# Kernel optimization log

Measured on AMD Instinct MI355X. Metric: run time of the kernel, lower is better.

## Reference

```python
import jax, jax.numpy as jnp
import numpy as np

TOPK = 2
NORM_TOPK = True
SCALE = 1.0
EPS = 1e-9


def setup_inputs() -> dict:
    key = jax.random.key(0)
    ks = jax.random.split(key, 9)
    h, i, E = 2048, 1024, 16
    std = 0.02
    return {
        "x": jax.random.normal(ks[0], (1, 2048, h), jnp.float32),
        "Wr": jax.random.normal(ks[1], (E, h), jnp.float32) * std,
        "bias": jnp.zeros((E,), jnp.float32),
        "Wg": jax.random.normal(ks[2], (E, h, i), jnp.float32) * std,
        "Wu": jax.random.normal(ks[3], (E, h, i), jnp.float32) * std,
        "Wd": jax.random.normal(ks[4], (E, i, h), jnp.float32) * std,
        "sWg": jax.random.normal(ks[5], (h, i), jnp.float32) * std,
        "sWu": jax.random.normal(ks[6], (h, i), jnp.float32) * std,
        "sWd": jax.random.normal(ks[7], (i, h), jnp.float32) * std,
    }


def reference(x, Wr, bias, Wg, Wu, Wd, sWg, sWu, sWd):
    b, s, h = x.shape
    E = Wr.shape[0]
    xt = x.reshape(b * s, h)  # [T, h]

    # Router: softmax over expert logits, then top-k
    logits = xt @ Wr.T + bias  # [T, E]
    probs = jax.nn.softmax(logits, axis=-1)
    topk_val, topk_idx = jax.lax.top_k(probs, TOPK)  # [T, K]
    if NORM_TOPK:
        w = topk_val / (jnp.sum(topk_val, axis=-1, keepdims=True) + EPS)
    else:
        w = topk_val
    w = w * SCALE

    # Dense per-expert SwiGLU (mathematically identical to gather/scatter dispatch)
    g = jnp.einsum('th,ehi->tei', xt, Wg)  # [T, E, i]
    u = jnp.einsum('th,ehi->tei', xt, Wu)
    y = jnp.einsum('tei,eih->teh', jax.nn.silu(g) * u, Wd)  # [T, E, h]

    # Combine: out[t] = sum_k w[t,k] * y[t, idx[t,k]]
    oh = jax.nn.one_hot(topk_idx, E, dtype=x.dtype)  # [T, K, E]
    routed = jnp.einsum('tke,tk,teh->th', oh, w, y)

    # Shared expert (SwiGLU)
    shared = (jax.nn.silu(xt @ sWg) * (xt @ sWu)) @ sWd

    return (routed + shared).reshape(b, s, h)
```

## Files before the change

kernel.cpp:

```cpp
#include <hip/hip_runtime.h>
#include <hip/hip_bf16.h>

#define T_TOK 2048
#define HDIM  2048
#define IDIM  1024
#define NE    16
#define NEX   17
#define NASSIGN (T_TOK*3)
#define TM    64

#define G1_NWG (TM*16)
#define G2_NWG (TM*32)

typedef __attribute__((ext_vector_type(8))) short bf16x8;
typedef __attribute__((ext_vector_type(4))) float f32x4;

#define WAITVM(N) asm volatile("s_waitcnt vmcnt(" #N ")" ::: "memory")
#define WAITLGKM0 asm volatile("s_waitcnt lgkmcnt(0)" ::: "memory")
#define SCHEDB    __builtin_amdgcn_sched_barrier(0)
#define BARRIER   __builtin_amdgcn_s_barrier()

__device__ __forceinline__ unsigned short f2bf(float f) {
    union { float f; unsigned u; } v; v.f = f;
    unsigned r = v.u + 0x7fffu + ((v.u >> 16) & 1u);
    return (unsigned short)(r >> 16);
}
__device__ __forceinline__ unsigned pack2f(float a, float b) {
    __hip_bfloat162 h = __float22bfloat162_rn(float2{a, b});
    unsigned r;
    __builtin_memcpy(&r, &h, 4);
    return r;
}
__device__ __forceinline__ int SW2(int r) { return (r >> 1) & 3; }
__device__ __forceinline__ int lds_off32(int row, int kelem) {
    return (row << 6) + ((((kelem >> 3) ^ SW2(row))) << 4) + ((kelem & 7) << 1);
}
__device__ __forceinline__ f32x4 mfma16(bf16x8 a, bf16x8 b, f32x4 c) {
    return __builtin_amdgcn_mfma_f32_16x16x32_bf16(a, b, c, 0, 0, 0);
}
__device__ __forceinline__ void gload_lds16(const void* g, void* lds) {
    __builtin_amdgcn_global_load_lds(
        (const __attribute__((address_space(1))) unsigned*)g,
        (__attribute__((address_space(3))) unsigned*)lds, 16, 0, 0);
}

__global__ __launch_bounds__(256) void k_cvt(const float* __restrict__ x,
                                             unsigned short* __restrict__ xbf) {
    int i = blockIdx.x * 256 + threadIdx.x;
    float4 v = ((const float4*)x)[i];
    uint2 p{pack2f(v.x, v.y), pack2f(v.z, v.w)};
    ((uint2*)xbf)[i] = p;
}

__global__ void k_router(const float* __restrict__ x, const float* __restrict__ Wr,
                         const float* __restrict__ bias, float* __restrict__ wtok,
                         int* __restrict__ idxtok, int* __restrict__ counts) {
    int t = blockIdx.x;
    int lane = threadIdx.x & 63;
    int wave = threadIdx.x >> 6;
    __shared__ float lg[NE];
    const float4* xr = (const float4*)(x + (size_t)t * HDIM);
    for (int e = wave; e < NE; e += 4) {
        const float4* wr = (const float4*)(Wr + (size_t)e * HDIM);
        float s = 0.f;
        for (int j = lane; j < HDIM / 4; j += 64) {
            float4 a = xr[j], b = wr[j];
            s += a.x*b.x + a.y*b.y + a.z*b.z + a.w*b.w;
        }
        #pragma unroll
        for (int d = 32; d; d >>= 1) s += __shfl_xor(s, d);
        if (lane == 0) lg[e] = s + bias[e];
    }
    __syncthreads();
    if (threadIdx.x == 0) {
        float m = lg[0];
        #pragma unroll
        for (int e = 1; e < NE; e++) m = fmaxf(m, lg[e]);
        float p[NE]; float S = 0.f;
        #pragma unroll
        for (int e = 0; e < NE; e++) { p[e] = expf(lg[e] - m); S += p[e]; }
        int i0 = 0;
        #pragma unroll
        for (int e = 1; e < NE; e++) if (p[e] > p[i0]) i0 = e;
        int i1 = (i0 == 0) ? 1 : 0;
        for (int e = 0; e < NE; e++) if (e != i0 && p[e] > p[i1]) i1 = e;
        float v0 = p[i0] / S, v1 = p[i1] / S;
        float wsum = v0 + v1 + 1e-9f;
        wtok[t*2+0] = v0 / wsum;
        wtok[t*2+1] = v1 / wsum;
        idxtok[t*2+0] = i0;
        idxtok[t*2+1] = i1;
        atomicAdd(&counts[i0], 1);
        atomicAdd(&counts[i1], 1);
    }
}

__global__ void k_scan(const int* __restrict__ counts, int* __restrict__ offs,
                       int* __restrict__ cursor, int4* __restrict__ tiles) {
    if (threadIdx.x == 0) {
        int acc = 0;
        for (int e = 0; e < NEX; e++) {
            offs[e] = acc; cursor[e] = acc;
            acc += (e < NE) ? counts[e] : T_TOK;
        }
        offs[NEX] = acc;
        int nt = 0;
        for (int e = 0; e < NEX; e++) {
            for (int r = offs[e]; r < offs[e+1]; r += 128) {
                tiles[nt] = int4{r, min(128, offs[e+1] - r), e, 0};
                nt++;
            }
        }
        for (; nt < TM; nt++) tiles[nt] = int4{0, 0, 0, 0};
    }
}

__global__ void k_scatter(const int* __restrict__ idxtok, const float* __restrict__ wtok,
                          int* __restrict__ cursor, const int* __restrict__ offs,
                          int* __restrict__ rows, float* __restrict__ wrow) {
    int t = blockIdx.x * blockDim.x + threadIdx.x;
    if (t >= T_TOK) return;
    #pragma unroll
    for (int k = 0; k < 2; k++) {
        int e = idxtok[t*2+k];
        int pos = atomicAdd(&cursor[e], 1);
        rows[pos] = t;
        wrow[pos] = wtok[t*2+k];
    }
    int p16 = offs[NE] + t;
    rows[p16] = t;
    wrow[p16] = 1.0f;
}

__global__ __launch_bounds__(512) void k_gemm1(
        const unsigned short* __restrict__ xbf,
        const float* __restrict__ Wg, const float* __restrict__ Wu,
        const float* __restrict__ sWg, const float* __restrict__ sWu,
        const int4* __restrict__ tiles, const int* __restrict__ rows,
        const float* __restrict__ wrow, unsigned short* __restrict__ act) {
    int bid = blockIdx.x;
    int wg = (bid & 7) * (G1_NWG >> 3) + (bid >> 3);
    int ti = wg & (TM - 1);
    int ct = wg >> 6;

    int4 tl = tiles[ti];
    int nrows = tl.y;
    if (nrows == 0) return;
    int rs = tl.x, e = tl.z;
    const float* wgp = (e < NE) ? Wg + (size_t)e * HDIM * IDIM : sWg;
    const float* wup = (e < NE) ? Wu + (size_t)e * HDIM * IDIM : sWu;
    int n0 = ct * 64;

    __shared__ unsigned short As[2][128 * 32];
    __shared__ unsigned short Bs[2][64 * 32];
    __shared__ unsigned short Us[2][64 * 32];

    int tid = threadIdx.x;
    int l = tid & 63, w = tid >> 6;

    int arow = w * 16 + (l >> 2);
    int rr = rows[rs + min(arow, nrows - 1)];
    const unsigned short* asrc = xbf + (size_t)rr * HDIM + (((l & 3) ^ SW2(arow)) << 3);

    int sm = tid >> 8;
    int sn = tid & 63;
    int skc = (tid >> 6) & 3;
    const float* wsrc = (sm ? wup : wgp) + (size_t)(skc * 8) * IDIM + n0 + sn;
    unsigned short* wdst0 = sm ? Us[0] : Bs[0];
    unsigned short* wdst1 = sm ? Us[1] : Bs[1];
    int swoff = lds_off32(sn, skc * 8);

    int wr = (w >> 2) << 6;
    int wc = (w & 3) << 4;
    int fr = l & 15;
    int fk = (l >> 4) << 3;

    float wA[8], wB[8];
    f32x4 accg[4] = {}, accu[4] = {};
    const int NK = HDIM / 32;

    #define G1_LOADW(DST, KS) do { \
        size_t kb_ = (size_t)(KS) * 32; \
        _Pragma("unroll") \
        for (int j = 0; j < 8; ++j) DST[j] = wsrc[(kb_ + j) * IDIM]; \
    } while (0)
    #define G1_WRITEW(SRC, P) do { \
        uint4 pw_; \
        pw_.x = pack2f(SRC[0], SRC[1]); pw_.y = pack2f(SRC[2], SRC[3]); \
        pw_.z = pack2f(SRC[4], SRC[5]); pw_.w = pack2f(SRC[6], SRC[7]); \
        *(uint4*)((char*)((P) ? wdst1 : wdst0) + swoff) = pw_; \
    } while (0)
    #define G1_MFMA(P) do { \
        bf16x8 a0 = *(const bf16x8*)((const char*)As[P] + lds_off32(wr + fr, fk)); \
        bf16x8 a1 = *(const bf16x8*)((const char*)As[P] + lds_off32(wr + 16 + fr, fk)); \
        bf16x8 a2 = *(const bf16x8*)((const char*)As[P] + lds_off32(wr + 32 + fr, fk)); \
        bf16x8 a3 = *(const bf16x8*)((const char*)As[P] + lds_off32(wr + 48 + fr, fk)); \
        bf16x8 bg = *(const bf16x8*)((const char*)Bs[P] + lds_off32(wc + fr, fk)); \
        bf16x8 bu = *(const bf16x8*)((const char*)Us[P] + lds_off32(wc + fr, fk)); \
        accg[0] = mfma16(a0, bg, accg[0]);  accu[0] = mfma16(a0, bu, accu[0]); \
        accg[1] = mfma16(a1, bg, accg[1]);  accu[1] = mfma16(a1, bu, accu[1]); \
        accg[2] = mfma16(a2, bg, accg[2]);  accu[2] = mfma16(a2, bu, accu[2]); \
        accg[3] = mfma16(a3, bg, accg[3]);  accu[3] = mfma16(a3, bu, accu[3]); \
    } while (0)
    #define G1_STEP(K, CUR, NXT, P) do { \
        gload_lds16(asrc + min((K) + 1, NK - 1) * 32, (char*)As[(P) ^ 1] + w * 1024); \
        SCHEDB; \
        G1_LOADW(NXT, min((K) + 2, NK - 1)); \
        SCHEDB; \
        WAITVM(9);               \
        G1_WRITEW(CUR, (P) ^ 1); \
        G1_MFMA(P); \
        SCHEDB; \
        WAITVM(8);               \
        WAITLGKM0; \
        BARRIER; \
        SCHEDB; \
    } while (0)

    G1_LOADW(wA, 0);
    gload_lds16(asrc, (char*)As[0] + w * 1024);
    SCHEDB;
    G1_LOADW(wB, 1);
    SCHEDB;
    WAITVM(9);
    G1_WRITEW(wA, 0);
    SCHEDB;
    WAITVM(8);
    WAITLGKM0;
    BARRIER;
    SCHEDB;

    for (int k = 0; k < NK; k += 2) {
        G1_STEP(k,     wB, wA, 0);
        G1_STEP(k + 1, wA, wB, 1);
    }
    asm volatile("s_waitcnt vmcnt(0)" ::: "memory");

    int crow = (l >> 4) << 2;
    int ccol = l & 15;
    #pragma unroll
    for (int m = 0; m < 4; ++m) {
        #pragma unroll
        for (int reg = 0; reg < 4; ++reg) {
            int r = wr + m * 16 + crow + reg;
            if (r < nrows) {
                float wv = wrow[rs + r];
                float g = accg[m][reg], u = accu[m][reg];
                act[(size_t)(rs + r) * IDIM + n0 + wc + ccol] =
                    f2bf(g / (1.f + __expf(-g)) * u * wv);
            }
        }
    }
    #undef G1_LOADW
    #undef G1_WRITEW
    #undef G1_MFMA
    #undef G1_STEP
}

__global__ __launch_bounds__(512) void k_gemm2(
        const unsigned short* __restrict__ act,
        const float* __restrict__ Wd, const float* __restrict__ sWd,
        const int4* __restrict__ tiles, const int* __restrict__ rows,
        float* __restrict__ out) {
    int bid = blockIdx.x;
    int wg = (bid & 7) * (G2_NWG >> 3) + (bid >> 3);
    int ti = wg & (TM - 1);
    int ct = wg >> 6;

    int4 tl = tiles[ti];
    int nrows = tl.y;
    if (nrows == 0) return;
    int rs = tl.x, e = tl.z;
    const float* wdp = (e < NE) ? Wd + (size_t)e * IDIM * HDIM : sWd;
    int n0 = ct * 64;

    __shared__ unsigned short As[2][128 * 32];
    __shared__ unsigned short Bs[2][64 * 32];

    int tid = threadIdx.x;
    int l = tid & 63, w = tid >> 6;

    int arow = w * 16 + (l >> 2);
    const unsigned short* asrc =
        act + (size_t)(rs + min(arow, nrows - 1)) * IDIM + (((l & 3) ^ SW2(arow)) << 3);

    int sn = tid & 63;
    int skc = (tid >> 6) & 7;
    const float* wsrc = wdp + (size_t)(skc * 4) * HDIM + n0 + sn;
    int swoff = lds_off32(sn, skc * 4);

    int wr = (w >> 2) << 6;
    int wc = (w & 3) << 4;
    int fr = l & 15;
    int fk = (l >> 4) << 3;

    float wA[4], wB[4];
    f32x4 acc[4] = {};
    const int NK = IDIM / 32;

    #define G2_LOADW(DST, KS) do { \
        size_t kb_ = (size_t)(KS) * 32; \
        _Pragma("unroll") \
        for (int j = 0; j < 4; ++j) DST[j] = wsrc[(kb_ + j) * HDIM]; \
    } while (0)
    #define G2_WRITEW(SRC, P) do { \
        uint2 pw_; \
        pw_.x = pack2f(SRC[0], SRC[1]); pw_.y = pack2f(SRC[2], SRC[3]); \
        *(uint2*)((char*)Bs[P] + swoff) = pw_; \
    } while (0)
    #define G2_MFMA(P) do { \
        bf16x8 a0 = *(const bf16x8*)((const char*)As[P] + lds_off32(wr + fr, fk)); \
        bf16x8 a1 = *(const bf16x8*)((const char*)As[P] + lds_off32(wr + 16 + fr, fk)); \
        bf16x8 a2 = *(const bf16x8*)((const char*)As[P] + lds_off32(wr + 32 + fr, fk)); \
        bf16x8 a3 = *(const bf16x8*)((const char*)As[P] + lds_off32(wr + 48 + fr, fk)); \
        bf16x8 b  = *(const bf16x8*)((const char*)Bs[P] + lds_off32(wc + fr, fk)); \
        acc[0] = mfma16(a0, b, acc[0]); \
        acc[1] = mfma16(a1, b, acc[1]); \
        acc[2] = mfma16(a2, b, acc[2]); \
        acc[3] = mfma16(a3, b, acc[3]); \
    } while (0)
    #define G2_STEP(K, CUR, NXT, P) do { \
        gload_lds16(asrc + min((K) + 1, NK - 1) * 32, (char*)As[(P) ^ 1] + w * 1024); \
        SCHEDB; \
        G2_LOADW(NXT, min((K) + 2, NK - 1)); \
        SCHEDB; \
        WAITVM(5); \
        G2_WRITEW(CUR, (P) ^ 1); \
        G2_MFMA(P); \
        SCHEDB; \
        WAITVM(4); \
        WAITLGKM0; \
        BARRIER; \
        SCHEDB; \
    } while (0)

    G2_LOADW(wA, 0);
    gload_lds16(asrc, (char*)As[0] + w * 1024);
    SCHEDB;
    G2_LOADW(wB, 1);
    SCHEDB;
    WAITVM(5);
    G2_WRITEW(wA, 0);
    SCHEDB;
    WAITVM(4);
    WAITLGKM0;
    BARRIER;
    SCHEDB;

    for (int k = 0; k < NK; k += 2) {
        G2_STEP(k,     wB, wA, 0);
        G2_STEP(k + 1, wA, wB, 1);
    }
    asm volatile("s_waitcnt vmcnt(0)" ::: "memory");

    int crow = (l >> 4) << 2;
    int ccol = l & 15;
    #pragma unroll
    for (int m = 0; m < 4; ++m) {
        #pragma unroll
        for (int reg = 0; reg < 4; ++reg) {
            int r = wr + m * 16 + crow + reg;
            if (r < nrows) {
                atomicAdd(&out[(size_t)rows[rs + r] * HDIM + n0 + wc + ccol], acc[m][reg]);
            }
        }
    }
    #undef G2_LOADW
    #undef G2_WRITEW
    #undef G2_MFMA
    #undef G2_STEP
}

extern "C" void kernel_launch(void* const* d_in, const int* in_sizes, int n_in,
                              void* d_out, int out_size, void* d_ws, size_t ws_size,
                              hipStream_t stream) {
    const float* x    = (const float*)d_in[0];
    const float* Wr   = (const float*)d_in[1];
    const float* bias = (const float*)d_in[2];
    const float* Wg   = (const float*)d_in[3];
    const float* Wu   = (const float*)d_in[4];
    const float* Wd   = (const float*)d_in[5];
    const float* sWg  = (const float*)d_in[6];
    const float* sWu  = (const float*)d_in[7];
    const float* sWd  = (const float*)d_in[8];
    float* out = (float*)d_out;

    char* p = (char*)d_ws;
    int*   counts = (int*)p;                 p += 256;
    int*   offs   = (int*)p;                 p += 256;
    int*   cursor = (int*)p;                 p += 256;
    int4*  tiles  = (int4*)p;                p += TM * sizeof(int4);
    int*   idxtok = (int*)p;                 p += (size_t)T_TOK * 2 * sizeof(int);
    float* wtok   = (float*)p;               p += (size_t)T_TOK * 2 * sizeof(float);
    int*   rows   = (int*)p;                 p += (size_t)NASSIGN * sizeof(int);
    float* wrow   = (float*)p;               p += (size_t)NASSIGN * sizeof(float);
    unsigned short* act = (unsigned short*)p; p += (size_t)NASSIGN * IDIM * sizeof(unsigned short);
    unsigned short* xbf = (unsigned short*)p;

    hipMemsetAsync(counts, 0, 256, stream);
    hipMemsetAsync(d_out, 0, (size_t)out_size * sizeof(float), stream);

    k_cvt<<<dim3(T_TOK * HDIM / 1024), dim3(256), 0, stream>>>(x, xbf);
    k_router<<<dim3(T_TOK), dim3(256), 0, stream>>>(x, Wr, bias, wtok, idxtok, counts);
    k_scan<<<dim3(1), dim3(64), 0, stream>>>(counts, offs, cursor, tiles);
    k_scatter<<<dim3((T_TOK + 255) / 256), dim3(256), 0, stream>>>(idxtok, wtok, cursor, offs, rows, wrow);
    k_gemm1<<<dim3(G1_NWG), dim3(512), 0, stream>>>(xbf, Wg, Wu, sWg, sWu, tiles, rows, wrow, act);
    k_gemm2<<<dim3(G2_NWG), dim3(512), 0, stream>>>(act, Wd, sWd, tiles, rows, out);
}
```

Before: 353.6 us.

## Double K-step to 64 and restructure load/MFMA pipeline in both MoE GEMMs

Measured after the change: 349.0 us. About the same (-1.3%).

```diff
diff --git a/kernel.cpp b/kernel.cpp
--- a/kernel.cpp
+++ b/kernel.cpp
@@ -151,9 +151,9 @@
     const float* wup = (e < NE) ? Wu + (size_t)e * HDIM * IDIM : sWu;
     int n0 = ct * 64;
 
-    __shared__ unsigned short As[2][128 * 32];
-    __shared__ unsigned short Bs[2][64 * 32];
-    __shared__ unsigned short Us[2][64 * 32];
+    __shared__ unsigned short As[2][8192];
+    __shared__ unsigned short Bs[4096];
+    __shared__ unsigned short Us[4096];
 
     int tid = threadIdx.x;
     int l = tid & 63, w = tid >> 6;
@@ -166,8 +166,7 @@
     int sn = tid & 63;
     int skc = (tid >> 6) & 3;
     const float* wsrc = (sm ? wup : wgp) + (size_t)(skc * 8) * IDIM + n0 + sn;
-    unsigned short* wdst0 = sm ? Us[0] : Bs[0];
-    unsigned short* wdst1 = sm ? Us[1] : Bs[1];
+    char* wdst = (char*)(sm ? Us : Bs);
     int swoff = lds_off32(sn, skc * 8);
 
     int wr = (w >> 2) << 6;
@@ -175,66 +174,86 @@
     int fr = l & 15;
     int fk = (l >> 4) << 3;
 
-    float wA[8], wB[8];
+    float wA[16], wB[16];
     f32x4 accg[4] = {}, accu[4] = {};
-    const int NK = HDIM / 32;
+    const int NK = HDIM / 64;
 
     #define G1_LOADW(DST, KS) do { \
-        size_t kb_ = (size_t)(KS) * 32; \
+        size_t kb_ = (size_t)(KS) * 64; \
         _Pragma("unroll") \
-        for (int j = 0; j < 8; ++j) DST[j] = wsrc[(kb_ + j) * IDIM]; \
-    } while (0)
-    #define G1_WRITEW(SRC, P) do { \
-        uint4 pw_; \
-        pw_.x = pack2f(SRC[0], SRC[1]); pw_.y = pack2f(SRC[2], SRC[3]); \
-        pw_.z = pack2f(SRC[4], SRC[5]); pw_.w = pack2f(SRC[6], SRC[7]); \
-        *(uint4*)((char*)((P) ? wdst1 : wdst0) + swoff) = pw_; \
+        for (int h = 0; h < 2; ++h) { \
+            _Pragma("unroll") \
+            for (int j = 0; j < 8; ++j) \
+                DST[h * 8 + j] = wsrc[(kb_ + h * 32 + j) * IDIM]; \
+        } \
+    } while (0)
+    #define G1_WRITEW(SRC) do { \
+        _Pragma("unroll") \
+        for (int h = 0; h < 2; ++h) { \
+            uint4 pw_; \
+            pw_.x = pack2f(SRC[h*8+0], SRC[h*8+1]); pw_.y = pack2f(SRC[h*8+2], SRC[h*8+3]); \
+            pw_.z = pack2f(SRC[h*8+4], SRC[h*8+5]); pw_.w = pack2f(SRC[h*8+6], SRC[h*8+7]); \
+            *(uint4*)(wdst + h * 4096 + swoff) = pw_; \
+        } \
+    } while (0)
+    #define G1_DMA(KS, P) do { \
+        gload_lds16(asrc + (size_t)(KS) * 64,      (char*)As[P] + w * 1024); \
+        gload_lds16(asrc + (size_t)(KS) * 64 + 32, (char*)As[P] + 8192 + w * 1024); \
     } while (0)
     #define G1_MFMA(P) do { \
-        bf16x8 a0 = *(const bf16x8*)((const char*)As[P] + lds_off32(wr + fr, fk)); \
-        bf16x8 a1 = *(const bf16x8*)((const char*)As[P] + lds_off32(wr + 16 + fr, fk)); \
-        bf16x8 a2 = *(const bf16x8*)((const char*)As[P] + lds_off32(wr + 32 + fr, fk)); \
-        bf16x8 a3 = *(const bf16x8*)((const char*)As[P] + lds_off32(wr + 48 + fr, fk)); \
-        bf16x8 bg = *(const bf16x8*)((const char*)Bs[P] + lds_off32(wc + fr, fk)); \
-        bf16x8 bu = *(const bf16x8*)((const char*)Us[P] + lds_off32(wc + fr, fk)); \
-        accg[0] = mfma16(a0, bg, accg[0]);  accu[0] = mfma16(a0, bu, accu[0]); \
-        accg[1] = mfma16(a1, bg, accg[1]);  accu[1] = mfma16(a1, bu, accu[1]); \
-        accg[2] = mfma16(a2, bg, accg[2]);  accu[2] = mfma16(a2, bu, accu[2]); \
-        accg[3] = mfma16(a3, bg, accg[3]);  accu[3] = mfma16(a3, bu, accu[3]); \
-    } while (0)
-    #define G1_STEP(K, CUR, NXT, P) do { \
-        gload_lds16(asrc + min((K) + 1, NK - 1) * 32, (char*)As[(P) ^ 1] + w * 1024); \
-        SCHEDB; \
-        G1_LOADW(NXT, min((K) + 2, NK - 1)); \
-        SCHEDB; \
-        WAITVM(9);               \
-        G1_WRITEW(CUR, (P) ^ 1); \
+        _Pragma("unroll") \
+        for (int kh = 0; kh < 2; ++kh) { \
+            const char* Ab = (const char*)As[P] + kh * 8192; \
+            const char* Bb = (const char*)Bs + kh * 4096; \
+            const char* Ub = (const char*)Us + kh * 4096; \
+            bf16x8 a0 = *(const bf16x8*)(Ab + lds_off32(wr + fr, fk)); \
+            bf16x8 a1 = *(const bf16x8*)(Ab + lds_off32(wr + 16 + fr, fk)); \
+            bf16x8 a2 = *(const bf16x8*)(Ab + lds_off32(wr + 32 + fr, fk)); \
+            bf16x8 a3 = *(const bf16x8*)(Ab + lds_off32(wr + 48 + fr, fk)); \
+            bf16x8 bg = *(const bf16x8*)(Bb + lds_off32(wc + fr, fk)); \
+            bf16x8 bu = *(const bf16x8*)(Ub + lds_off32(wc + fr, fk)); \
+            accg[0] = mfma16(a0, bg, accg[0]);  accu[0] = mfma16(a0, bu, accu[0]); \
+            accg[1] = mfma16(a1, bg, accg[1]);  accu[1] = mfma16(a1, bu, accu[1]); \
+            accg[2] = mfma16(a2, bg, accg[2]);  accu[2] = mfma16(a2, bu, accu[2]); \
+            accg[3] = mfma16(a3, bg, accg[3]);  accu[3] = mfma16(a3, bu, accu[3]); \
+        } \
+    } while (0)
+    #define G1_STEP(K, CUR, P) do { \
         G1_MFMA(P); \
         SCHEDB; \
-        WAITVM(8);               \
+        BARRIER; \
+        SCHEDB; \
+        G1_DMA(min((K) + 2, NK - 1), P); \
+        G1_WRITEW(CUR); \
+        SCHEDB; \
+        WAITVM(2);             \
+        G1_LOADW(CUR, min((K) + 3, NK - 1)); \
+        SCHEDB; \
         WAITLGKM0; \
         BARRIER; \
         SCHEDB; \
     } while (0)
 
     G1_LOADW(wA, 0);
-    gload_lds16(asrc, (char*)As[0] + w * 1024);
-    SCHEDB;
+    G1_DMA(0, 0);
     G1_LOADW(wB, 1);
     SCHEDB;
-    WAITVM(9);
-    G1_WRITEW(wA, 0);
-    SCHEDB;
-    WAITVM(8);
+    WAITVM(18);
+    G1_WRITEW(wA);
+    G1_DMA(1, 1);
+    SCHEDB;
+    WAITVM(2);
+    G1_LOADW(wA, 2);
+    SCHEDB;
     WAITLGKM0;
     BARRIER;
     SCHEDB;
 
     for (int k = 0; k < NK; k += 2) {
-        G1_STEP(k,     wB, wA, 0);
-        G1_STEP(k + 1, wA, wB, 1);
-    }
-    asm volatile("s_waitcnt vmcnt(0)" ::: "memory");
+        G1_STEP(k,     wB, 0);
+        G1_STEP(k + 1, wA, 1);
+    }
+    WAITVM(0);
 
     int crow = (l >> 4) << 2;
     int ccol = l & 15;
@@ -253,6 +272,7 @@
     }
     #undef G1_LOADW
     #undef G1_WRITEW
+    #undef G1_DMA
     #undef G1_MFMA
     #undef G1_STEP
 }
@@ -274,8 +294,8 @@
     const float* wdp = (e < NE) ? Wd + (size_t)e * IDIM * HDIM : sWd;
     int n0 = ct * 64;
 
-    __shared__ unsigned short As[2][128 * 32];
-    __shared__ unsigned short Bs[2][64 * 32];
+    __shared__ unsigned short As[2][8192];
+    __shared__ unsigned short Bs[4096];
 
     int tid = threadIdx.x;
     int l = tid & 63, w = tid >> 6;
@@ -286,72 +306,85 @@
 
     int sn = tid & 63;
     int skc = (tid >> 6) & 7;
-    const float* wsrc = wdp + (size_t)(skc * 4) * HDIM + n0 + sn;
-    int swoff = lds_off32(sn, skc * 4);
+    const float* wsrc = wdp + (size_t)(skc * 8) * HDIM + n0 + sn;
+    int swoff = ((skc >> 2) * 4096) + lds_off32(sn, (skc & 3) * 8);
 
     int wr = (w >> 2) << 6;
     int wc = (w & 3) << 4;
     int fr = l & 15;
     int fk = (l >> 4) << 3;
 
-    float wA[4], wB[4];
+    float wA[8], wB[8];
     f32x4 acc[4] = {};
-    const int NK = IDIM / 32;
+    const int NK = IDIM / 64;
 
     #define G2_LOADW(DST, KS) do { \
-        size_t kb_ = (size_t)(KS) * 32; \
+        size_t kb_ = (size_t)(KS) * 64; \
         _Pragma("unroll") \
-        for (int j = 0; j < 4; ++j) DST[j] = wsrc[(kb_ + j) * HDIM]; \
-    } while (0)
-    #define G2_WRITEW(SRC, P) do { \
-        uint2 pw_; \
+        for (int j = 0; j < 8; ++j) DST[j] = wsrc[(kb_ + j) * HDIM]; \
+    } while (0)
+    #define G2_WRITEW(SRC) do { \
+        uint4 pw_; \
         pw_.x = pack2f(SRC[0], SRC[1]); pw_.y = pack2f(SRC[2], SRC[3]); \
-        *(uint2*)((char*)Bs[P] + swoff) = pw_; \
+        pw_.z = pack2f(SRC[4], SRC[5]); pw_.w = pack2f(SRC[6], SRC[7]); \
+        *(uint4*)((char*)Bs + swoff) = pw_; \
+    } while (0)
+    #define G2_DMA(KS, P) do { \
+        gload_lds16(asrc + (size_t)(KS) * 64,      (char*)As[P] + w * 1024); \
+        gload_lds16(asrc + (size_t)(KS) * 64 + 32, (char*)As[P] + 8192 + w * 1024); \
     } while (0)
     #define G2_MFMA(P) do { \
-        bf16x8 a0 = *(const bf16x8*)((const char*)As[P] + lds_off32(wr + fr, fk)); \
-        bf16x8 a1 = *(const bf16x8*)((const char*)As[P] + lds_off32(wr + 16 + fr, fk)); \
-        bf16x8 a2 = *(const bf16x8*)((const char*)As[P] + lds_off32(wr + 32 + fr, fk)); \
-        bf16x8 a3 = *(const bf16x8*)((const char*)As[P] + lds_off32(wr + 48 + fr, fk)); \
-        bf16x8 b  = *(const bf16x8*)((const char*)Bs[P] + lds_off32(wc + fr, fk)); \
-        acc[0] = mfma16(a0, b, acc[0]); \
-        acc[1] = mfma16(a1, b, acc[1]); \
-        acc[2] = mfma16(a2, b, acc[2]); \
-        acc[3] = mfma16(a3, b, acc[3]); \
-    } while (0)
-    #define G2_STEP(K, CUR, NXT, P) do { \
-        gload_lds16(asrc + min((K) + 1, NK - 1) * 32, (char*)As[(P) ^ 1] + w * 1024); \
-        SCHEDB; \
-        G2_LOADW(NXT, min((K) + 2, NK - 1)); \
-        SCHEDB; \
-        WAITVM(5); \
-        G2_WRITEW(CUR, (P) ^ 1); \
+        _Pragma("unroll") \
+        for (int kh = 0; kh < 2; ++kh) { \
+            const char* Ab = (const char*)As[P] + kh * 8192; \
+            const char* Bb = (const char*)Bs + kh * 4096; \
+            bf16x8 a0 = *(const bf16x8*)(Ab + lds_off32(wr + fr, fk)); \
+            bf16x8 a1 = *(const bf16x8*)(Ab + lds_off32(wr + 16 + fr, fk)); \
+            bf16x8 a2 = *(const bf16x8*)(Ab + lds_off32(wr + 32 + fr, fk)); \
+            bf16x8 a3 = *(const bf16x8*)(Ab + lds_off32(wr + 48 + fr, fk)); \
+            bf16x8 b  = *(const bf16x8*)(Bb + lds_off32(wc + fr, fk)); \
+            acc[0] = mfma16(a0, b, acc[0]); \
+            acc[1] = mfma16(a1, b, acc[1]); \
+            acc[2] = mfma16(a2, b, acc[2]); \
+            acc[3] = mfma16(a3, b, acc[3]); \
+        } \
+    } while (0)
+    #define G2_STEP(K, CUR, P) do { \
         G2_MFMA(P); \
         SCHEDB; \
-        WAITVM(4); \
+        BARRIER; \
+        SCHEDB; \
+        G2_DMA(min((K) + 2, NK - 1), P); \
+        G2_WRITEW(CUR); \
+        SCHEDB; \
+        WAITVM(2); \
+        G2_LOADW(CUR, min((K) + 3, NK - 1)); \
+        SCHEDB; \
         WAITLGKM0; \
         BARRIER; \
         SCHEDB; \
     } while (0)
 
     G2_LOADW(wA, 0);
-    gload_lds16(asrc, (char*)As[0] + w * 1024);
-    SCHEDB;
+    G2_DMA(0, 0);
     G2_LOADW(wB, 1);
     SCHEDB;
-    WAITVM(5);
-    G2_WRITEW(wA, 0);
-    SCHEDB;
-    WAITVM(4);
+    WAITVM(10);
+    G2_WRITEW(wA);
+    G2_DMA(1, 1);
+    SCHEDB;
+    WAITVM(2);
+    G2_LOADW(wA, 2);
+    SCHEDB;
     WAITLGKM0;
     BARRIER;
     SCHEDB;
 
     for (int k = 0; k < NK; k += 2) {
-        G2_STEP(k,     wB, wA, 0);
-        G2_STEP(k + 1, wA, wB, 1);
-    }
-    asm volatile("s_waitcnt vmcnt(0)" ::: "memory");
+        G2_STEP(k,     wB, 0);
+        G2_STEP(k + 1, wA, 1);
+    }
+    WAITVM(0);
 
     int crow = (l >> 4) << 2;
     int ccol = l & 15;
@@ -367,6 +400,7 @@
     }
     #undef G2_LOADW
     #undef G2_WRITEW
+    #undef G2_DMA
     #undef G2_MFMA
     #undef G2_STEP
 }
```
